# Optimization experiments

Measured on AMD Instinct MI355X. Metric: run time of the kernel, lower is better.

Reference implementation:

```python
import jax, jax.numpy as jnp
import numpy as np

N = 50000      # nodes
E = 800000     # edges
IN = 64        # in_channels
HID = 16       # hidden_channels
HEADS = 4
HC = HID * HEADS  # 64 == IN, so all 3 layers share in-dim 64
EDIM = 16
L = 3
G = 2000       # graphs
BN_EPS = 1e-5


def setup_inputs() -> dict:
    key = jax.random.key(0)
    ks = jax.random.split(key, 24)
    inp = {
        "x": jax.random.normal(ks[0], (N, IN), jnp.float32),
        "edge_index": jax.random.randint(ks[1], (2, E), 0, N, jnp.int64),
        "edge_attr": jax.random.normal(ks[2], (E, EDIM), jnp.float32),
        "batch": jnp.sort(jax.random.randint(ks[3], (N,), 0, G, jnp.int64)),
    }
    s = 0.05
    # stacked per-layer TransformerConv params (all layers have in-dim 64)
    inp["Wq"] = jax.random.normal(ks[4], (L, HC, HC), jnp.float32) * s
    inp["bq"] = jnp.zeros((L, HC), jnp.float32)
    inp["Wk"] = jax.random.normal(ks[5], (L, HC, HC), jnp.float32) * s
    inp["bk"] = jnp.zeros((L, HC), jnp.float32)
    inp["Wv"] = jax.random.normal(ks[6], (L, HC, HC), jnp.float32) * s
    inp["bv"] = jnp.zeros((L, HC), jnp.float32)
    inp["We"] = jax.random.normal(ks[7], (L, EDIM, HC), jnp.float32) * s  # lin_edge, no bias
    inp["Ws"] = jax.random.normal(ks[8], (L, HC, HC), jnp.float32) * s   # lin_skip
    inp["bs"] = jnp.zeros((L, HC), jnp.float32)
    # BatchNorm1d (eval mode) per layer
    inp["bn_g"] = jnp.ones((L, HC), jnp.float32)
    inp["bn_b"] = jnp.zeros((L, HC), jnp.float32)
    inp["bn_m"] = jax.random.normal(ks[9], (L, HC), jnp.float32) * 0.01
    inp["bn_v"] = 0.5 + jax.random.uniform(ks[10], (L, HC), jnp.float32)
    # head MLP
    inp["fc1_w"] = jax.random.normal(ks[11], (HC, HID), jnp.float32) * s
    inp["fc1_b"] = jnp.zeros((HID,), jnp.float32)
    inp["fc2_w"] = jax.random.normal(ks[12], (HID, 1), jnp.float32) * s
    inp["fc2_b"] = jnp.zeros((1,), jnp.float32)
    return inp


def _segment_softmax(logits, seg, n):
    # logits: [E, H]; softmax over edges sharing the same target node
    m = jax.ops.segment_max(logits, seg, num_segments=n)       # [N, H]
    ex = jnp.exp(logits - m[seg])
    den = jax.ops.segment_sum(ex, seg, num_segments=n)         # [N, H]
    return ex / den[seg]


def _transformer_conv(x, src, dst, edge_attr, Wq, bq, Wk, bk, Wv, bv, We, Ws, bs):
    n = x.shape[0]
    q = (x @ Wq + bq).reshape(n, HEADS, HID)[dst]              # [E, H, C]
    e_emb = (edge_attr @ We).reshape(-1, HEADS, HID)           # [E, H, C]
    k = (x @ Wk + bk).reshape(n, HEADS, HID)[src] + e_emb
    v = (x @ Wv + bv).reshape(n, HEADS, HID)[src] + e_emb
    logits = jnp.sum(q * k, axis=-1) / jnp.sqrt(jnp.asarray(HID, x.dtype))  # [E, H]
    alpha = _segment_softmax(logits, dst, n)
    agg = jax.ops.segment_sum(alpha[..., None] * v, dst, num_segments=n)    # [N, H, C]
    return agg.reshape(n, HC) + x @ Ws + bs


def reference(x, edge_index, edge_attr, batch, Wq, bq, Wk, bk, Wv, bv, We, Ws, bs,
              bn_g, bn_b, bn_m, bn_v, fc1_w, fc1_b, fc2_w, fc2_b):
    src, dst = edge_index[0], edge_index[1]
    for l in range(Wq.shape[0]):
        x = _transformer_conv(x, src, dst, edge_attr,
                              Wq[l], bq[l], Wk[l], bk[l], Wv[l], bv[l],
                              We[l], Ws[l], bs[l])
        x = jax.nn.relu((x - bn_m[l]) * jax.lax.rsqrt(bn_v[l] + BN_EPS) * bn_g[l] + bn_b[l])
        # dropout is identity in eval / p given at init
    counts = jax.ops.segment_sum(jnp.ones((x.shape[0],), x.dtype), batch, num_segments=G)
    pooled = jax.ops.segment_sum(x, batch, num_segments=G) / jnp.maximum(counts, 1.0)[:, None]
    h = jax.nn.relu(pooled @ fc1_w + fc1_b)
    return h @ fc2_w + fc2_b
```

## Files before the change

kernel.cpp:

```cpp
#include <hip/hip_runtime.h>
#include <math.h>

#define N_NODES 50000
#define N_EDGES 800000
#define HC 64
#define HID 16
#define EDIM 16
#define NGRAPH 2000
#define BN_EPS 1e-5f
#define QKVS_NODES 32
#define XSP 68
#define SCAN_NBLK ((N_NODES + 255) / 256)
#define SCAT_BLOCKS 1024
#define NODES_PER_CLS (N_NODES / 8)

typedef __attribute__((ext_vector_type(2))) float v2f;
__device__ inline float4 fp8x4_to_f4(unsigned w) {
    v2f lo = __builtin_amdgcn_cvt_pk_f32_fp8((int)w, false);
    v2f hi = __builtin_amdgcn_cvt_pk_f32_fp8((int)w, true);
    return make_float4(lo[0], lo[1], hi[0], hi[1]);
}
__device__ inline unsigned char f2fp8(float f) {
    int r = __builtin_amdgcn_cvt_pk_fp8_f32(f, f, 0, false);
    return (unsigned char)(r & 0xff);
}
__device__ inline unsigned short f2bf(float f) {
    union { float f; unsigned u; } v; v.f = f;
    unsigned r = v.u + 0x7fffu + ((v.u >> 16) & 1u);
    return (unsigned short)(r >> 16);
}
__device__ inline float4 bf4_to_f4(uint2 r) {
    float4 o;
    o.x = __uint_as_float(r.x << 16);
    o.y = __uint_as_float(r.x & 0xffff0000u);
    o.z = __uint_as_float(r.y << 16);
    o.w = __uint_as_float(r.y & 0xffff0000u);
    return o;
}

__global__ void count_deg(const int* __restrict__ ei, int* __restrict__ deg) {
    int e = blockIdx.x * blockDim.x + threadIdx.x;
    if (e < N_EDGES) atomicAdd(&deg[ei[N_EDGES + e]], 1);
}

__global__ __launch_bounds__(256) void scan1(const int* __restrict__ deg, int* __restrict__ bsum) {
    __shared__ int s[256];
    int tid = threadIdx.x;
    int i = blockIdx.x * 256 + tid;
    s[tid] = (i < N_NODES) ? deg[i] : 0;
    __syncthreads();
    for (int d = 128; d > 0; d >>= 1) {
        if (tid < d) s[tid] += s[tid + d];
        __syncthreads();
    }
    if (tid == 0) bsum[blockIdx.x] = s[0];
}

__global__ __launch_bounds__(256) void scan3(const int* __restrict__ deg, const int* __restrict__ bsum,
                                             int* __restrict__ row_ptr, int* __restrict__ nxt) {
    __shared__ int s[256];
    __shared__ int boff_s;
    int tid = threadIdx.x;
    int v2 = (tid < SCAN_NBLK) ? bsum[tid] : 0;
    s[tid] = v2;
    __syncthreads();
    for (int d = 1; d < 256; d <<= 1) {
        int t = (tid >= d) ? s[tid - d] : 0;
        __syncthreads();
        s[tid] += t;
        __syncthreads();
    }
    if (tid == (int)blockIdx.x) boff_s = s[tid] - v2;
    __syncthreads();
    int i = blockIdx.x * 256 + tid;
    int v = (i < N_NODES) ? deg[i] : 0;
    s[tid] = v;
    __syncthreads();
    for (int d = 1; d < 256; d <<= 1) {
        int t = (tid >= d) ? s[tid - d] : 0;
        __syncthreads();
        s[tid] += t;
        __syncthreads();
    }
    int excl = s[tid] - v + boff_s;
    if (i < N_NODES) { row_ptr[i] = excl; nxt[i] = excl; }
    if (i == 0) row_ptr[N_NODES] = N_EDGES;
}

__global__ __launch_bounds__(256) void scatter_edges(const int* __restrict__ ei,
                                                     int* __restrict__ next_ptr,
                                                     int2* __restrict__ se_s) {
    int cls = blockIdx.x & 7;
    int nodeLo = cls * NODES_PER_CLS;
    int nodeHi = nodeLo + NODES_PER_CLS;
    int stride = (SCAT_BLOCKS >> 3) * 256;
    int e = (blockIdx.x >> 3) * 256 + threadIdx.x;
    for (; e < N_EDGES; e += stride) {
        int d = __builtin_nontemporal_load(ei + N_EDGES + e);
        if (d >= nodeLo && d < nodeHi) {
            int s = __builtin_nontemporal_load(ei + e);
            int p = atomicAdd(&next_ptr[d], 1);
            se_s[p] = make_int2(s, e);
        }
    }
}

__global__ __launch_bounds__(256) void qkvs_kernel(
    const float* __restrict__ x,
    const float* __restrict__ Wq, const float* __restrict__ bq,
    const float* __restrict__ Wk, const float* __restrict__ bk,
    const float* __restrict__ Wv, const float* __restrict__ bv,
    const float* __restrict__ Ws, const float* __restrict__ bs,
    const float* __restrict__ We,
    unsigned short* __restrict__ Qo, unsigned char* __restrict__ KVo,
    unsigned short* __restrict__ So, unsigned short* __restrict__ qwe_buf) {
    __shared__ float xs[QKVS_NODES][XSP];
    int tid = threadIdx.x;
    int n0 = blockIdx.x * QKVS_NODES;
    for (int c = tid; c < QKVS_NODES * HC / 4; c += 256) {
        int row = c >> 4, col4 = c & 15;
        int n = n0 + row;
        float4 v = (n < N_NODES) ? ((const float4*)(x + (size_t)n * HC))[col4]
                                 : make_float4(0.f, 0.f, 0.f, 0.f);
        *(float4*)&xs[row][col4 * 4] = v;
    }
    __syncthreads();
    int sel = tid >> 6;
    int t = tid & 63;
    int j4 = (t & 15) * 4;
    int ng = t >> 4;
    const float* W; const float* B;
    if (sel == 0)      { W = Wq; B = bq; }
    else if (sel == 1) { W = Wk; B = bk; }
    else if (sel == 2) { W = Wv; B = bv; }
    else               { W = Ws; B = bs; }
    float4 b4 = *(const float4*)(B + j4);
    float acc[8][4];
#pragma unroll
    for (int n = 0; n < 8; n++) {
        acc[n][0] = b4.x; acc[n][1] = b4.y; acc[n][2] = b4.z; acc[n][3] = b4.w;
    }
    for (int i4 = 0; i4 < HC / 4; i4++) {
        float4 w0 = *(const float4*)(W + (i4 * 4 + 0) * HC + j4);
        float4 w1 = *(const float4*)(W + (i4 * 4 + 1) * HC + j4);
        float4 w2 = *(const float4*)(W + (i4 * 4 + 2) * HC + j4);
        float4 w3 = *(const float4*)(W + (i4 * 4 + 3) * HC + j4);
#pragma unroll
        for (int n = 0; n < 8; n++) {
            float4 xv = *(const float4*)&xs[ng + 4 * n][i4 * 4];
            acc[n][0] = fmaf(xv.x, w0.x, acc[n][0]);
            acc[n][0] = fmaf(xv.y, w1.x, acc[n][0]);
            acc[n][0] = fmaf(xv.z, w2.x, acc[n][0]);
            acc[n][0] = fmaf(xv.w, w3.x, acc[n][0]);
            acc[n][1] = fmaf(xv.x, w0.y, acc[n][1]);
            acc[n][1] = fmaf(xv.y, w1.y, acc[n][1]);
            acc[n][1] = fmaf(xv.z, w2.y, acc[n][1]);
            acc[n][1] = fmaf(xv.w, w3.y, acc[n][1]);
            acc[n][2] = fmaf(xv.x, w0.z, acc[n][2]);
            acc[n][2] = fmaf(xv.y, w1.z, acc[n][2]);
            acc[n][2] = fmaf(xv.z, w2.z, acc[n][2]);
            acc[n][2] = fmaf(xv.w, w3.z, acc[n][2]);
            acc[n][3] = fmaf(xv.x, w0.w, acc[n][3]);
            acc[n][3] = fmaf(xv.y, w1.w, acc[n][3]);
            acc[n][3] = fmaf(xv.z, w2.w, acc[n][3]);
            acc[n][3] = fmaf(xv.w, w3.w, acc[n][3]);
        }
    }
    if (sel == 0 || sel == 3) {
        unsigned short* Out = (sel == 0) ? Qo : So;
#pragma unroll
        for (int n = 0; n < 8; n++) {
            int node = n0 + ng + 4 * n;
            if (node < N_NODES) {
                ushort4 pk;
                pk.x = f2bf(acc[n][0]); pk.y = f2bf(acc[n][1]);
                pk.z = f2bf(acc[n][2]); pk.w = f2bf(acc[n][3]);
                *(ushort4*)(Out + (size_t)node * HC + j4) = pk;
            }
        }
    } else {
        int off = (sel == 1) ? 0 : HC;
#pragma unroll
        for (int n = 0; n < 8; n++) {
            int node = n0 + ng + 4 * n;
            if (node < N_NODES) {
                uchar4 pk;
                pk.x = f2fp8(acc[n][0]); pk.y = f2fp8(acc[n][1]);
                pk.z = f2fp8(acc[n][2]); pk.w = f2fp8(acc[n][3]);
                *(uchar4*)(KVo + (size_t)node * 2 * HC + off + j4) = pk;
            }
        }
    }

    __syncthreads();
    if (sel == 0) {
#pragma unroll
        for (int n = 0; n < 8; n++)
            *(float4*)&xs[ng + 4 * n][j4] =
                make_float4(acc[n][0], acc[n][1], acc[n][2], acc[n][3]);
    }
    __syncthreads();
    {
        int j = tid & 63;
        int h2 = j >> 4, jj = j & 15;
        float4 wv0 = *(const float4*)(We + jj * HC + h2 * 16 + 0);
        float4 wv1 = *(const float4*)(We + jj * HC + h2 * 16 + 4);
        float4 wv2 = *(const float4*)(We + jj * HC + h2 * 16 + 8);
        float4 wv3 = *(const float4*)(We + jj * HC + h2 * 16 + 12);
#pragma unroll
        for (int n = 0; n < 8; n++) {
            int nn = sel * 8 + n;
            float4 q0 = *(const float4*)&xs[nn][h2 * 16 + 0];
            float4 q1 = *(const float4*)&xs[nn][h2 * 16 + 4];
            float4 q2 = *(const float4*)&xs[nn][h2 * 16 + 8];
            float4 q3 = *(const float4*)&xs[nn][h2 * 16 + 12];
            float s = q0.x * wv0.x + q0.y * wv0.y + q0.z * wv0.z + q0.w * wv0.w
                    + q1.x * wv1.x + q1.y * wv1.y + q1.z * wv1.z + q1.w * wv1.w
                    + q2.x * wv2.x + q2.y * wv2.y + q2.z * wv2.z + q2.w * wv2.w
                    + q3.x * wv3.x + q3.y * wv3.y + q3.z * wv3.z + q3.w * wv3.w;
            int node = n0 + nn;
            if (node < N_NODES) qwe_buf[(size_t)node * HC + j] = f2bf(s);
        }
    }
}

__global__ __launch_bounds__(256) void attn_kernel(
    const unsigned short* __restrict__ Qf, const unsigned short* __restrict__ Qwe,
    const unsigned char* __restrict__ KV, const unsigned short* __restrict__ Sf,
    const int* __restrict__ row_ptr, const int2* __restrict__ se_s,
    const float* __restrict__ edge_attr, const float* __restrict__ We,
    const float* __restrict__ bng, const float* __restrict__ bnb,
    const float* __restrict__ bnm, const float* __restrict__ bnv,
    float* __restrict__ x_out) {
    __shared__ float we_s[EDIM * HC];
    int tid = threadIdx.x;
    for (int c = tid; c < EDIM * HC / 4; c += 256)
        ((float4*)we_s)[c] = ((const float4*)We)[c];
    __syncthreads();

    int lane = tid & 63;
    int wave = tid >> 6;
    int half = lane >> 5;
    int node = blockIdx.x * 8 + wave * 2 + half;
    int sub = (lane >> 4) & 1;
    int pos = lane & 15;
    int h = pos >> 2;
    int eaIdx = pos & 3;
    int rbeg = row_ptr[node], rend = row_ptr[node + 1];

    float4 q4 = bf4_to_f4(((const uint2*)(Qf + (size_t)node * HC))[pos]);
    float4 qwe = bf4_to_f4(((const uint2*)(Qwe + (size_t)node * HC))[pos]);

    float den = 0.f;
    float4 acc = make_float4(0.f, 0.f, 0.f, 0.f);
    float4 aea = make_float4(0.f, 0.f, 0.f, 0.f);

    auto proc = [&](float4 k4, float4 ea4) -> float {
        float dot = q4.x * k4.x + q4.y * k4.y + q4.z * k4.z + q4.w * k4.w
                  + qwe.x * ea4.x + qwe.y * ea4.y + qwe.z * ea4.z + qwe.w * ea4.w;
        dot += __shfl_xor(dot, 1);
        dot += __shfl_xor(dot, 2);
        float p = __expf(dot * 0.25f);
        den += p;
        return p;
    };
    auto accum = [&](float p, const float4& v, const float4& ea) {
        acc.x = fmaf(p, v.x, acc.x); acc.y = fmaf(p, v.y, acc.y);
        acc.z = fmaf(p, v.z, acc.z); acc.w = fmaf(p, v.w, acc.w);
        aea.x = fmaf(p, ea.x, aea.x); aea.y = fmaf(p, ea.y, aea.y);
        aea.z = fmaf(p, ea.z, aea.z); aea.w = fmaf(p, ea.w, aea.w);
    };

    int j = rbeg + sub;
    for (; j + 2 < rend; j += 4) {
        int2 se0 = se_s[j];
        int2 se1 = se_s[j + 2];
        const unsigned int* kv0 = (const unsigned int*)(KV + (size_t)se0.x * 2 * HC);
        const unsigned int* kv1 = (const unsigned int*)(KV + (size_t)se1.x * 2 * HC);
        unsigned int k0w = kv0[pos], v0w = kv0[16 + pos];
        unsigned int k1w = kv1[pos], v1w = kv1[16 + pos];
        float4 ea0 = ((const float4*)(edge_attr + (size_t)se0.y * EDIM))[eaIdx];
        float4 ea1 = ((const float4*)(edge_attr + (size_t)se1.y * EDIM))[eaIdx];
        float4 k0 = fp8x4_to_f4(k0w), v0 = fp8x4_to_f4(v0w);
        float4 k1 = fp8x4_to_f4(k1w), v1 = fp8x4_to_f4(v1w);
        float p0 = proc(k0, ea0);
        accum(p0, v0, ea0);
        float p1 = proc(k1, ea1);
        accum(p1, v1, ea1);
    }
    if (j < rend) {
        int2 se0 = se_s[j];
        const unsigned int* kv0 = (const unsigned int*)(KV + (size_t)se0.x * 2 * HC);
        unsigned int k0w = kv0[pos], v0w = kv0[16 + pos];
        float4 ea0 = ((const float4*)(edge_attr + (size_t)se0.y * EDIM))[eaIdx];
        float4 k0 = fp8x4_to_f4(k0w), v0 = fp8x4_to_f4(v0w);
        float p0 = proc(k0, ea0);
        accum(p0, v0, ea0);
    }

    {
        den += __shfl_xor(den, 16);
        acc.x += __shfl_xor(acc.x, 16); acc.y += __shfl_xor(acc.y, 16);
        acc.z += __shfl_xor(acc.z, 16); acc.w += __shfl_xor(acc.w, 16);
        aea.x += __shfl_xor(aea.x, 16); aea.y += __shfl_xor(aea.y, 16);
        aea.z += __shfl_xor(aea.z, 16); aea.w += __shfl_xor(aea.w, 16);
    }

    float4 e4 = make_float4(0.f, 0.f, 0.f, 0.f);
#pragma unroll
    for (int jg = 0; jg < 4; jg++) {
        int sl = (lane & 32) | (h * 4 + jg);
        float a0 = __shfl(aea.x, sl), a1 = __shfl(aea.y, sl);
        float a2 = __shfl(aea.z, sl), a3 = __shfl(aea.w, sl);
        float4 w0 = *(const float4*)(we_s + (jg * 4 + 0) * HC + pos * 4);
        float4 w1 = *(const float4*)(we_s + (jg * 4 + 1) * HC + pos * 4);
        float4 w2 = *(const float4*)(we_s + (jg * 4 + 2) * HC + pos * 4);
        float4 w3 = *(const float4*)(we_s + (jg * 4 + 3) * HC + pos * 4);
        e4.x += a0 * w0.x + a1 * w1.x + a2 * w2.x + a3 * w3.x;
        e4.y += a0 * w0.y + a1 * w1.y + a2 * w2.y + a3 * w3.y;
        e4.z += a0 * w0.z + a1 * w1.z + a2 * w2.z + a3 * w3.z;
        e4.w += a0 * w0.w + a1 * w1.w + a2 * w2.w + a3 * w3.w;
    }

    float inv = (rend > rbeg) ? 1.f / den : 0.f;
    float4 sk = bf4_to_f4(((const uint2*)(Sf + (size_t)node * HC))[pos]);
    float4 o = make_float4((acc.x + e4.x) * inv + sk.x, (acc.y + e4.y) * inv + sk.y,
                           (acc.z + e4.z) * inv + sk.z, (acc.w + e4.w) * inv + sk.w);
    float4 g4 = ((const float4*)bng)[pos];
    float4 b4 = ((const float4*)bnb)[pos];
    float4 m4 = ((const float4*)bnm)[pos];
    float4 vv4 = ((const float4*)bnv)[pos];
    o.x = fmaxf((o.x - m4.x) * rsqrtf(vv4.x + BN_EPS) * g4.x + b4.x, 0.f);
    o.y = fmaxf((o.y - m4.y) * rsqrtf(vv4.y + BN_EPS) * g4.y + b4.y, 0.f);
    o.z = fmaxf((o.z - m4.z) * rsqrtf(vv4.z + BN_EPS) * g4.z + b4.z, 0.f);
    o.w = fmaxf((o.w - m4.w) * rsqrtf(vv4.w + BN_EPS) * g4.w + b4.w, 0.f);
    if (sub == 0) ((float4*)(x_out + (size_t)node * HC))[pos] = o;
}

__global__ __launch_bounds__(256) void pool_head(
    const float* __restrict__ x, const int* __restrict__ batch,
    const float* __restrict__ fc1_w, const float* __restrict__ fc1_b,
    const float* __restrict__ fc2_w, const float* __restrict__ fc2_b,
    float* __restrict__ out) {
    __shared__ float ps[4][HC];
    int q = threadIdx.x >> 6;
    int lane = threadIdx.x & 63;
    int g = blockIdx.x * 4 + q;
    int lo = 0, hi = N_NODES;
    while (lo < hi) { int mid = (lo + hi) >> 1; if (batch[mid] < g) lo = mid + 1; else hi = mid; }
    int beg = lo;
    lo = 0; hi = N_NODES;
    while (lo < hi) { int mid = (lo + hi) >> 1; if (batch[mid] < g + 1) lo = mid + 1; else hi = mid; }
    int end = lo;
    float s = 0.f;
    for (int i = beg; i < end; i++) s += x[(size_t)i * HC + lane];
    float inv = (end > beg) ? 1.f / (float)(end - beg) : 1.f;
    ps[q][lane] = s * inv;
    __syncthreads();
    float o = 0.f;
    if (lane < HID) {
        float a = fc1_b[lane];
#pragma unroll
        for (int i = 0; i < HC; i++) a = fmaf(ps[q][i], fc1_w[i * HID + lane], a);
        o = fmaxf(a, 0.f) * fc2_w[lane];
    }
    o += __shfl_xor(o, 1);
    o += __shfl_xor(o, 2);
    o += __shfl_xor(o, 4);
    o += __shfl_xor(o, 8);
    if (lane == 0) out[g] = o + fc2_b[0];
}

extern "C" void kernel_launch(void* const* d_in, const int* in_sizes, int n_in,
                              void* d_out, int out_size, void* d_ws, size_t ws_size,
                              hipStream_t stream) {
    const float* x         = (const float*)d_in[0];
    const int*   ei        = (const int*)d_in[1];
    const float* edge_attr = (const float*)d_in[2];
    const int*   batch     = (const int*)d_in[3];
    const float* Wq = (const float*)d_in[4];  const float* bq = (const float*)d_in[5];
    const float* Wk = (const float*)d_in[6];  const float* bk = (const float*)d_in[7];
    const float* Wv = (const float*)d_in[8];  const float* bv = (const float*)d_in[9];
    const float* We = (const float*)d_in[10];
    const float* Ws = (const float*)d_in[11]; const float* bs = (const float*)d_in[12];
    const float* bng = (const float*)d_in[13]; const float* bnb = (const float*)d_in[14];
    const float* bnm = (const float*)d_in[15]; const float* bnv = (const float*)d_in[16];
    const float* fc1_w = (const float*)d_in[17]; const float* fc1_b = (const float*)d_in[18];
    const float* fc2_w = (const float*)d_in[19]; const float* fc2_b = (const float*)d_in[20];
    float* out = (float*)d_out;

    char* wp = (char*)d_ws;
    auto alloc = [&](size_t b) { void* p = (void*)wp; wp += (b + 255) & ~(size_t)255; return p; };
    float* xA      = (float*)alloc((size_t)N_NODES * HC * 4);
    float* xB      = (float*)alloc((size_t)N_NODES * HC * 4);
    unsigned short* Qb   = (unsigned short*)alloc((size_t)N_NODES * HC * 2);
    unsigned short* Sb   = (unsigned short*)alloc((size_t)N_NODES * HC * 2);
    unsigned char*  KV   = (unsigned char*)alloc((size_t)N_NODES * 2 * HC);
    unsigned short* qweb = (unsigned short*)alloc((size_t)N_NODES * HC * 2);
    int*   deg     = (int*)alloc((size_t)N_NODES * 4);
    int*   row_ptr = (int*)alloc((size_t)(N_NODES + 1) * 4);
    int*   nxt     = (int*)alloc((size_t)N_NODES * 4);
    int*   bsum    = (int*)alloc((size_t)256 * 4);
    int2*  se_s    = (int2*)alloc((size_t)N_EDGES * 8);

    (void)hipMemsetAsync(deg, 0, (size_t)N_NODES * 4, stream);

    count_deg<<<(N_EDGES + 255) / 256, 256, 0, stream>>>(ei, deg);
    scan1<<<SCAN_NBLK, 256, 0, stream>>>(deg, bsum);
    scan3<<<SCAN_NBLK, 256, 0, stream>>>(deg, bsum, row_ptr, nxt);
    scatter_edges<<<SCAT_BLOCKS, 256, 0, stream>>>(ei, nxt, se_s);

    const float* xin = x;
    float* bufs[2] = {xA, xB};
    for (int l = 0; l < 3; l++) {
        float* xout = bufs[l & 1];
        qkvs_kernel<<<(N_NODES + QKVS_NODES - 1) / QKVS_NODES, 256, 0, stream>>>(
            xin, Wq + l * HC * HC, bq + l * HC, Wk + l * HC * HC, bk + l * HC,
            Wv + l * HC * HC, bv + l * HC, Ws + l * HC * HC, bs + l * HC,
            We + l * EDIM * HC, Qb, KV, Sb, qweb);
        attn_kernel<<<N_NODES / 8, 256, 0, stream>>>(
            Qb, qweb, KV, Sb, row_ptr, se_s, edge_attr, We + l * EDIM * HC,
            bng + l * HC, bnb + l * HC, bnm + l * HC, bnv + l * HC, xout);
        xin = xout;
    }
    pool_head<<<NGRAPH / 4, 256, 0, stream>>>(xin, batch, fc1_w, fc1_b, fc2_w, fc2_b, out);
}
```

Before: 446.9 us.

## Pre-permute edge attributes into CSR order as bf16 during edge scatter

The edge scatter kernel now reads each edge's 16 float attributes, converts them to bf16 and writes them contiguously at the edge's sorted CSR position, alongside a separate source-index array. The attention kernel then reads attributes sequentially by CSR index instead of gathering fp32 rows by original edge id in each of the three layers. This trades a one-time extra pass and bf16 rounding of edge attributes for halved, coalesced edge-attribute traffic in every layer.

```diff
diff --git a/kernel.cpp b/kernel.cpp
--- a/kernel.cpp
+++ b/kernel.cpp
@@ -29,6 +29,9 @@
     unsigned r = v.u + 0x7fffu + ((v.u >> 16) & 1u);
     return (unsigned short)(r >> 16);
 }
+__device__ inline unsigned pk2bf(float a, float b) {
+    return (unsigned)f2bf(a) | ((unsigned)f2bf(b) << 16);
+}
 __device__ inline float4 bf4_to_f4(uint2 r) {
     float4 o;
     o.x = __uint_as_float(r.x << 16);
@@ -88,8 +91,10 @@
 }
 
 __global__ __launch_bounds__(256) void scatter_edges(const int* __restrict__ ei,
+                                                     const float* __restrict__ edge_attr,
                                                      int* __restrict__ next_ptr,
-                                                     int2* __restrict__ se_s) {
+                                                     int* __restrict__ src_s,
+                                                     unsigned short* __restrict__ ea_s) {
     int cls = blockIdx.x & 7;
     int nodeLo = cls * NODES_PER_CLS;
     int nodeHi = nodeLo + NODES_PER_CLS;
@@ -100,7 +105,19 @@
         if (d >= nodeLo && d < nodeHi) {
             int s = __builtin_nontemporal_load(ei + e);
             int p = atomicAdd(&next_ptr[d], 1);
-            se_s[p] = make_int2(s, e);
+            src_s[p] = s;
+            const float* a = edge_attr + (size_t)e * EDIM;
+            float4 a0 = *(const float4*)(a + 0);
+            float4 a1 = *(const float4*)(a + 4);
+            float4 a2 = *(const float4*)(a + 8);
+            float4 a3 = *(const float4*)(a + 12);
+            uint4 w0, w1;
+            w0.x = pk2bf(a0.x, a0.y); w0.y = pk2bf(a0.z, a0.w);
+            w0.z = pk2bf(a1.x, a1.y); w0.w = pk2bf(a1.z, a1.w);
+            w1.x = pk2bf(a2.x, a2.y); w1.y = pk2bf(a2.z, a2.w);
+            w1.z = pk2bf(a3.x, a3.y); w1.w = pk2bf(a3.z, a3.w);
+            uint4* dst = (uint4*)(ea_s + (size_t)p * EDIM);
+            dst[0] = w0; dst[1] = w1;
         }
     }
 }
@@ -227,8 +244,8 @@
 __global__ __launch_bounds__(256) void attn_kernel(
     const unsigned short* __restrict__ Qf, const unsigned short* __restrict__ Qwe,
     const unsigned char* __restrict__ KV, const unsigned short* __restrict__ Sf,
-    const int* __restrict__ row_ptr, const int2* __restrict__ se_s,
-    const float* __restrict__ edge_attr, const float* __restrict__ We,
+    const int* __restrict__ row_ptr, const int* __restrict__ src_s,
+    const unsigned short* __restrict__ ea_s, const float* __restrict__ We,
     const float* __restrict__ bng, const float* __restrict__ bnb,
     const float* __restrict__ bnm, const float* __restrict__ bnv,
     float* __restrict__ x_out) {
@@ -273,14 +290,14 @@
 
     int j = rbeg + sub;
     for (; j + 2 < rend; j += 4) {
-        int2 se0 = se_s[j];
-        int2 se1 = se_s[j + 2];
-        const unsigned int* kv0 = (const unsigned int*)(KV + (size_t)se0.x * 2 * HC);
-        const unsigned int* kv1 = (const unsigned int*)(KV + (size_t)se1.x * 2 * HC);
+        int s0 = src_s[j];
+        int s1 = src_s[j + 2];
+        const unsigned int* kv0 = (const unsigned int*)(KV + (size_t)s0 * 2 * HC);
+        const unsigned int* kv1 = (const unsigned int*)(KV + (size_t)s1 * 2 * HC);
         unsigned int k0w = kv0[pos], v0w = kv0[16 + pos];
         unsigned int k1w = kv1[pos], v1w = kv1[16 + pos];
-        float4 ea0 = ((const float4*)(edge_attr + (size_t)se0.y * EDIM))[eaIdx];
-        float4 ea1 = ((const float4*)(edge_attr + (size_t)se1.y * EDIM))[eaIdx];
+        float4 ea0 = bf4_to_f4(((const uint2*)(ea_s + (size_t)j * EDIM))[eaIdx]);
+        float4 ea1 = bf4_to_f4(((const uint2*)(ea_s + (size_t)(j + 2) * EDIM))[eaIdx]);
         float4 k0 = fp8x4_to_f4(k0w), v0 = fp8x4_to_f4(v0w);
         float4 k1 = fp8x4_to_f4(k1w), v1 = fp8x4_to_f4(v1w);
         float p0 = proc(k0, ea0);
@@ -289,10 +306,10 @@
         accum(p1, v1, ea1);
     }
     if (j < rend) {
-        int2 se0 = se_s[j];
-        const unsigned int* kv0 = (const unsigned int*)(KV + (size_t)se0.x * 2 * HC);
+        int s0 = src_s[j];
+        const unsigned int* kv0 = (const unsigned int*)(KV + (size_t)s0 * 2 * HC);
         unsigned int k0w = kv0[pos], v0w = kv0[16 + pos];
-        float4 ea0 = ((const float4*)(edge_attr + (size_t)se0.y * EDIM))[eaIdx];
+        float4 ea0 = bf4_to_f4(((const uint2*)(ea_s + (size_t)j * EDIM))[eaIdx]);
         float4 k0 = fp8x4_to_f4(k0w), v0 = fp8x4_to_f4(v0w);
         float p0 = proc(k0, ea0);
         accum(p0, v0, ea0);
@@ -401,14 +418,15 @@
     int*   row_ptr = (int*)alloc((size_t)(N_NODES + 1) * 4);
     int*   nxt     = (int*)alloc((size_t)N_NODES * 4);
     int*   bsum    = (int*)alloc((size_t)256 * 4);
-    int2*  se_s    = (int2*)alloc((size_t)N_EDGES * 8);
+    int*   src_s   = (int*)alloc((size_t)N_EDGES * 4);
+    unsigned short* ea_s = (unsigned short*)alloc((size_t)N_EDGES * EDIM * 2);
 
     (void)hipMemsetAsync(deg, 0, (size_t)N_NODES * 4, stream);
 
     count_deg<<<(N_EDGES + 255) / 256, 256, 0, stream>>>(ei, deg);
     scan1<<<SCAN_NBLK, 256, 0, stream>>>(deg, bsum);
     scan3<<<SCAN_NBLK, 256, 0, stream>>>(deg, bsum, row_ptr, nxt);
-    scatter_edges<<<SCAT_BLOCKS, 256, 0, stream>>>(ei, nxt, se_s);
+    scatter_edges<<<SCAT_BLOCKS, 256, 0, stream>>>(ei, edge_attr, nxt, src_s, ea_s);
 
     const float* xin = x;
     float* bufs[2] = {xA, xB};
@@ -419,7 +437,7 @@
             Wv + l * HC * HC, bv + l * HC, Ws + l * HC * HC, bs + l * HC,
             We + l * EDIM * HC, Qb, KV, Sb, qweb);
         attn_kernel<<<N_NODES / 8, 256, 0, stream>>>(
-            Qb, qweb, KV, Sb, row_ptr, se_s, edge_attr, We + l * EDIM * HC,
+            Qb, qweb, KV, Sb, row_ptr, src_s, ea_s, We + l * EDIM * HC,
             bng + l * HC, bnb + l * HC, bnm + l * HC, bnv + l * HC, xout);
         xin = xout;
     }
```

New measurement: 464.0 us. +3.8%, slower.
